# Performance work log

Hardware: AMD Instinct MI355X
Metric: run time of the kernel (lower is better)

## Reference

```python
import jax, jax.numpy as jnp
import numpy as np

B, T, D_IN, D_OUT = 4, 2048, 1024, 1024


def setup_inputs() -> dict:
    key = jax.random.key(0)
    k1, k2, k3, k4 = jax.random.split(key, 4)
    s_in = 1.0 / np.sqrt(D_IN)
    return {
        "input_vector": jax.random.normal(k1, (B, T, D_IN), dtype=jnp.float32),
        "w_q": jax.random.normal(k2, (D_IN, D_OUT), dtype=jnp.float32) * s_in,
        "w_k": jax.random.normal(k3, (D_IN, D_OUT), dtype=jnp.float32) * s_in,
        "w_v": jax.random.normal(k4, (D_IN, D_OUT), dtype=jnp.float32) * s_in,
    }


def reference(input_vector, w_q, w_k, w_v):
    # projections: [B, T, D_OUT]
    q = jnp.einsum("btd,de->bte", input_vector, w_q)
    k = jnp.einsum("btd,de->bte", input_vector, w_k)
    v = jnp.einsum("btd,de->bte", input_vector, w_v)

    T_ = q.shape[1]
    # raw scores [B, T, T]
    scores = jnp.einsum("bqd,bkd->bqk", q, k)
    # causal mask (strict upper triangle masked to -inf), applied BEFORE scaling
    # (as in the original; -inf is invariant under the scale anyway)
    causal = jnp.tril(jnp.ones((T_, T_), dtype=bool))  # True = keep
    scores = jnp.where(causal[None, :, :], scores, -jnp.inf)
    scores = scores / jnp.sqrt(jnp.asarray(k.shape[-1], scores.dtype))
    attn = jax.nn.softmax(scores, axis=-1)
    # dropout = 0.0 (eval): identity
    return jnp.einsum("bqk,bkd->bqd", attn, v)
```

## Files before the change

kernel.cpp:

```cpp
#include <hip/hip_runtime.h>
#include <cstdint>

typedef unsigned short u16;
typedef __attribute__((ext_vector_type(8))) short short8;
typedef __attribute__((ext_vector_type(16))) float f32x16;

__device__ __forceinline__ u16 f2bf(float f) {
  uint32_t u = __float_as_uint(f);
  u += 0x7FFFu + ((u >> 16) & 1u);
  return (u16)(u >> 16);
}

__device__ __forceinline__ void async_ld16(u16* lds, const u16* g) {
  __builtin_amdgcn_global_load_lds((const __attribute__((address_space(1))) uint32_t*)g,
                                   (__attribute__((address_space(3))) uint32_t*)lds,
                                   16, 0, 0);
}

__device__ __forceinline__ void lgkm0_fence() {
  asm volatile("s_waitcnt lgkmcnt(0)" ::: "memory");
  __builtin_amdgcn_sched_barrier(0);
}
__device__ __forceinline__ void vmw6_fence() {
  asm volatile("s_waitcnt vmcnt(6)" ::: "memory");
  __builtin_amdgcn_sched_barrier(0);
}
__device__ __forceinline__ void vmw0_fence() {
  asm volatile("s_waitcnt vmcnt(0)" ::: "memory");
  __builtin_amdgcn_sched_barrier(0);
}

#define MFMA32 __builtin_amdgcn_mfma_f32_32x32x16_bf16

template <int ROLE>
__global__ __launch_bounds__(512, 2) void g8(
    const u16* __restrict__ Xbf, const u16* __restrict__ Wt,
    u16* __restrict__ QK, u16* __restrict__ VtAll,
    u16* __restrict__ P, float* __restrict__ lpart)
{
  const int b = blockIdx.x;
  const int tid = threadIdx.x;
  const int lane = tid & 63;
  const int wave = tid >> 6;
  const int wr2 = wave >> 2;
  const int wc2 = wave & 3;
  const int m32 = lane & 31;
  const int hh = lane >> 5;

  __shared__ __align__(16) u16 ls[2][2][16384];

  const u16 *Abase, *Bh0, *Bh1;
  int m0, n0, zb = 0;
  bool scoresRole = false;

  if constexpr (ROLE == 0) {
    m0 = (b >> 3) * 256;
    n0 = (b & 7) * 128;
    Abase = Xbf;
    Bh0 = Wt;
    Bh1 = Wt + 1024L * 1024;
  } else {
    if (b < 144) {
      scoresRole = true;
      zb = b / 36;
      const int w = b - zb * 36;
      int mt = 0;
      while ((mt + 1) * (mt + 2) / 2 <= w) ++mt;
      const int nt = w - mt * (mt + 1) / 2;
      m0 = nt * 256;
      n0 = mt * 256;
      Abase = QK + 8192L * 1024 + (long)zb * 2048 * 1024;
      const u16* Bq = QK + (long)zb * 2048 * 1024;
      Bh0 = Bq; Bh1 = Bq;
    } else {
      const int v = b - 144;
      m0 = (v >> 5) * 256;
      n0 = (v & 31) * 256;
      Abase = Wt + 2L * 1024 * 1024;
      Bh0 = Xbf; Bh1 = Xbf;
    }
  }

  const int sr = tid >> 3, sg = tid & 7;
  const long swz = (long)((sg ^ (sr & 7)) * 8);
  const u16* pAst = Abase + (long)(m0 + sr) * 1024 + swz;
  const u16* pB[2];
  if constexpr (ROLE == 0) {
    pB[0] = Bh0 + (long)(n0 + sr) * 1024 + swz;
    pB[1] = Bh1 + (long)(n0 + sr) * 1024 + swz;
  } else {
    pB[0] = Bh0 + (long)(n0 + sr) * 1024 + swz;
    pB[1] = Bh0 + (long)(n0 + 128 + sr) * 1024 + swz;
  }

#define STG_A(bf, h, t_) do { \
    u16* _d = &ls[bf][0][(h) * 8192] + tid * 8; \
    const u16* _s = pAst + (long)(h) * 131072 + (long)(t_) * 64; \
    async_ld16(_d, _s); async_ld16(_d + 4096, _s + 65536); } while (0)
#define STG_B(bf, h, t_) do { \
    u16* _d = &ls[bf][1][(h) * 8192] + tid * 8; \
    const u16* _s = pB[h] + (long)(t_) * 64; \
    async_ld16(_d, _s); async_ld16(_d + 4096, _s + 65536); } while (0)

  int offAk[4], offBk[2][4];
#pragma unroll
  for (int ks = 0; ks < 4; ++ks) {
    const int kq = ((ks << 1) | hh) ^ (m32 & 7);
    offAk[ks] = (wr2 * 128 + m32) * 64 + kq * 8;
#pragma unroll
    for (int j = 0; j < 2; ++j) {
      const int rowB = (ROLE == 0) ? (j * 128 + wc2 * 32 + m32)
                                   : (wc2 * 64 + j * 32 + m32);
      offBk[j][ks] = rowB * 64 + kq * 8;
    }
  }

  f32x16 acc[4][2];
#pragma unroll
  for (int i = 0; i < 4; ++i)
#pragma unroll
    for (int j = 0; j < 2; ++j)
#pragma unroll
      for (int r = 0; r < 16; ++r) acc[i][j][r] = 0.f;

  STG_A(0, 0, 0); STG_A(0, 1, 0); STG_B(0, 0, 0); STG_B(0, 1, 0);
  STG_B(1, 0, 1); STG_B(1, 1, 1); STG_A(1, 0, 1);
  vmw6_fence();
  __builtin_amdgcn_s_barrier();

  short8 A0[4], A1[4], A2[4], A3[4], B0r[4], B1r[4];

#pragma unroll 1
  for (int t = 0; t < 16; ++t) {
    const u16* la = ls[t & 1][0];
    const u16* lb = ls[t & 1][1];

#pragma unroll
    for (int ks = 0; ks < 4; ++ks) {
      A0[ks]  = *(const short8*)&la[offAk[ks]];
      A1[ks]  = *(const short8*)&la[offAk[ks] + 2048];
      B0r[ks] = *(const short8*)&lb[offBk[0][ks]];
    }
    if (t < 15) STG_A((t + 1) & 1, 1, t + 1);
    __builtin_amdgcn_s_barrier();
    lgkm0_fence();
    __builtin_amdgcn_s_setprio(1);
#pragma unroll
    for (int ks = 0; ks < 4; ++ks) {
      acc[0][0] = MFMA32(A0[ks], B0r[ks], acc[0][0], 0, 0, 0);
      acc[1][0] = MFMA32(A1[ks], B0r[ks], acc[1][0], 0, 0, 0);
    }
    __builtin_amdgcn_s_setprio(0);
    __builtin_amdgcn_s_barrier();

#pragma unroll
    for (int ks = 0; ks < 4; ++ks)
      B1r[ks] = *(const short8*)&lb[offBk[1][ks]];
    __builtin_amdgcn_s_barrier();
    lgkm0_fence();
    __builtin_amdgcn_s_setprio(1);
#pragma unroll
    for (int ks = 0; ks < 4; ++ks) {
      acc[0][1] = MFMA32(A0[ks], B1r[ks], acc[0][1], 0, 0, 0);
      acc[1][1] = MFMA32(A1[ks], B1r[ks], acc[1][1], 0, 0, 0);
    }
    __builtin_amdgcn_s_setprio(0);
    __builtin_amdgcn_s_barrier();

#pragma unroll
    for (int ks = 0; ks < 4; ++ks) {
      A2[ks] = *(const short8*)&la[offAk[ks] + 4096];
      A3[ks] = *(const short8*)&la[offAk[ks] + 6144];
    }
    if (t < 14) STG_B(t & 1, 0, t + 2);
    __builtin_amdgcn_s_barrier();
    lgkm0_fence();
    __builtin_amdgcn_s_setprio(1);
#pragma unroll
    for (int ks = 0; ks < 4; ++ks) {
      acc[2][0] = MFMA32(A2[ks], B0r[ks], acc[2][0], 0, 0, 0);
      acc[3][0] = MFMA32(A3[ks], B0r[ks], acc[3][0], 0, 0, 0);
    }
    __builtin_amdgcn_s_setprio(0);
    __builtin_amdgcn_s_barrier();

    if (t < 14) { STG_B(t & 1, 1, t + 2); STG_A(t & 1, 0, t + 2); }
    __builtin_amdgcn_s_barrier();
    __builtin_amdgcn_s_setprio(1);
#pragma unroll
    for (int ks = 0; ks < 4; ++ks) {
      acc[2][1] = MFMA32(A2[ks], B1r[ks], acc[2][1], 0, 0, 0);
      acc[3][1] = MFMA32(A3[ks], B1r[ks], acc[3][1], 0, 0, 0);
    }
    __builtin_amdgcn_s_setprio(0);
    if (t < 14) vmw6_fence(); else vmw0_fence();
    __builtin_amdgcn_s_barrier();
  }
#undef STG_A
#undef STG_B

  const int ec = lane & 31;
  const int rb = hh * 4;

  if constexpr (ROLE == 0) {
#pragma unroll
    for (int j = 0; j < 2; ++j) {
      u16* Cj = QK + (long)j * 8192 * 1024;
      const int col = n0 + wc2 * 32 + ec;
#pragma unroll
      for (int i = 0; i < 4; ++i) {
        const int rbase = m0 + wr2 * 128 + i * 32 + rb;
#pragma unroll
        for (int r = 0; r < 16; ++r) {
          const int row = rbase + (r & 3) + 8 * (r >> 2);
          Cj[(long)row * 1024 + col] = f2bf(acc[i][j][r]);
        }
      }
    }
  } else if (scoresRole) {
    u16* Pp = P + (long)zb * 2048 * 2048;
    float* lpz = lpart + (long)zb * 16 * 2048;
    const int chunk = (m0 >> 7) + wr2;
#pragma unroll
    for (int j = 0; j < 2; ++j) {
      const int q = n0 + wc2 * 64 + j * 32 + ec;
      float s = 0.f;
#pragma unroll
      for (int i = 0; i < 4; ++i) {
        const int kb = m0 + wr2 * 128 + i * 32 + rb;
#pragma unroll
        for (int u = 0; u < 4; ++u) {
          const int k0r = kb + u * 8;
          float pv[4];
#pragma unroll
          for (int v = 0; v < 4; ++v) {
            float e = __expf(acc[i][j][u * 4 + v] * 0.03125f);
            if (k0r + v > q) e = 0.f;
            pv[v] = e;
            s += e;
          }
          ushort4 o;
          o.x = f2bf(pv[0]); o.y = f2bf(pv[1]);
          o.z = f2bf(pv[2]); o.w = f2bf(pv[3]);
          *(ushort4*)&Pp[(long)q * 2048 + k0r] = o;
        }
      }
      s += __shfl_xor(s, 32, 64);
      if (hh == 0) lpz[(long)chunk * 2048 + q] = s;
    }
  } else {
#pragma unroll
    for (int i = 0; i < 4; ++i) {
      const int rbase = m0 + wr2 * 128 + i * 32 + rb;
#pragma unroll
      for (int j = 0; j < 2; ++j) {
        const int col = n0 + wc2 * 64 + j * 32 + ec;
#pragma unroll
        for (int r = 0; r < 16; ++r) {
          const int row = rbase + (r & 3) + 8 * (r >> 2);
          VtAll[(long)row * 8192 + col] = f2bf(acc[i][j][r]);
        }
      }
    }
  }
}

__global__ __launch_bounds__(256) void pv(
    const u16* __restrict__ VtAll, const u16* __restrict__ P,
    const float* __restrict__ lpart, float* __restrict__ out)
{
  const int b = blockIdx.x;
  const int tid = threadIdx.x;
  const int lane = tid & 63;
  const int wave = tid >> 6;
  const int wr = (wave >> 1) * 64;
  const int wc = (wave & 1) * 32;

  __shared__ __align__(16) u16 lsa[2][4096];
  __shared__ __align__(16) u16 lsb[2][2048];
  __shared__ float l_s[128];

  const int zb = blockIdx.y;
  const int mb = 15 - (b >> 4);
  const int nb = b & 15;
  const int m0 = mb * 128;
  const int n0 = nb * 64;
  const int kmax = (mb + 1) * 128;

  const u16* A = P + (long)zb * 2048 * 2048;
  const u16* B = VtAll + (long)zb * 2048;

  const int c0 = tid, c1 = tid + 256;
  const int r0 = c0 >> 2, q0 = ((c0 & 3) ^ ((c0 >> 3) & 3)) * 8;
  const int r1 = c1 >> 2, q1 = ((c1 & 3) ^ ((c1 >> 3) & 3)) * 8;

  const int m32 = lane & 31;
  const int hh = lane >> 5;
  const int rsw = (m32 >> 1) & 3;
  int offA[2][2], offB[2];
#pragma unroll
  for (int ks = 0; ks < 2; ++ks) {
    const int kq = ((ks << 1) | hh) ^ rsw;
#pragma unroll
    for (int i = 0; i < 2; ++i)
      offA[i][ks] = (wr + i * 32 + m32) * 32 + kq * 8;
    offB[ks] = (wc + m32) * 32 + kq * 8;
  }

  const u16* pA0 = A + (long)(m0 + r0) * 2048 + q0;
  const u16* pA1 = A + (long)(m0 + r1) * 2048 + q1;
  const u16* pB0 = B + (long)(n0 + r0) * 8192 + q0;

  f32x16 acc[2];
#pragma unroll
  for (int i = 0; i < 2; ++i)
#pragma unroll
    for (int r = 0; r < 16; ++r) acc[i][r] = 0.f;

  async_ld16(&lsa[0][c0 * 8], pA0);
  async_ld16(&lsa[0][c1 * 8], pA1);
  async_ld16(&lsb[0][c0 * 8], pB0);
  pA0 += 32; pA1 += 32; pB0 += 32;

  int p = 0;
  for (int k0 = 0; k0 < kmax; k0 += 32) {
    __syncthreads();
    if (k0 + 32 < kmax) {
      async_ld16(&lsa[p ^ 1][c0 * 8], pA0);
      async_ld16(&lsa[p ^ 1][c1 * 8], pA1);
      async_ld16(&lsb[p ^ 1][c0 * 8], pB0);
      pA0 += 32; pA1 += 32; pB0 += 32;
    }
    const u16* la = lsa[p];
    const u16* lb = lsb[p];
#pragma unroll
    for (int ks = 0; ks < 2; ++ks) {
      const short8 a0 = *(const short8*)&la[offA[0][ks]];
      const short8 a1 = *(const short8*)&la[offA[1][ks]];
      const short8 bb = *(const short8*)&lb[offB[ks]];
      acc[0] = MFMA32(a0, bb, acc[0], 0, 0, 0);
      acc[1] = MFMA32(a1, bb, acc[1], 0, 0, 0);
    }
    p ^= 1;
  }

  __syncthreads();
  if (tid < 128) {
    const float* lp = lpart + (long)zb * 16 * 2048 + m0 + tid;
    float s = 0.f;
    const int nch = (mb | 1) + 1;
    for (int c = 0; c < nch; ++c) s += lp[(long)c * 2048];
    l_s[tid] = 1.f / s;
  }
  __syncthreads();

  const int ec = lane & 31;
  const int rb = hh * 4;
  float* Cf = out + (long)zb * 2048 * 1024;
#pragma unroll
  for (int i = 0; i < 2; ++i) {
    const int rbl = wr + i * 32 + rb;
    const int col = n0 + wc + ec;
#pragma unroll
    for (int r = 0; r < 16; ++r) {
      const int rl = rbl + (r & 3) + 8 * (r >> 2);
      Cf[(long)(m0 + rl) * 1024 + col] = acc[i][r] * l_s[rl];
    }
  }
}

__global__ __launch_bounds__(256) void cast_fused(
    const float* __restrict__ x, const float* __restrict__ w0,
    const float* __restrict__ w1, const float* __restrict__ w2,
    u16* __restrict__ Xbf, u16* __restrict__ Wt)
{
  const int b = blockIdx.x;
  if (b < 8192) {
    const long i = ((long)b * 256 + threadIdx.x) * 4;
    const float4 v = *(const float4*)(x + i);
    ushort4 o;
    o.x = f2bf(v.x); o.y = f2bf(v.y); o.z = f2bf(v.z); o.w = f2bf(v.w);
    *(ushort4*)(Xbf + i) = o;
  } else {
    const int bb = b - 8192;
    const int z = bb >> 10, rem = bb & 1023;
    const float* W = (z == 0) ? w0 : (z == 1) ? w1 : w2;
    u16* o = Wt + (long)z * 1024 * 1024;
    __shared__ float t[32][33];
    const int n0 = (rem & 31) * 32, k0 = (rem >> 5) * 32;
    const int tx = threadIdx.x & 31, ty = threadIdx.x >> 5;
    for (int r = ty; r < 32; r += 8) t[r][tx] = W[(long)(k0 + r) * 1024 + n0 + tx];
    __syncthreads();
    for (int r = ty; r < 32; r += 8) o[(long)(n0 + r) * 1024 + k0 + tx] = f2bf(t[tx][r]);
  }
}

extern "C" void kernel_launch(void* const* d_in, const int* in_sizes, int n_in,
                              void* d_out, int out_size, void* d_ws, size_t ws_size,
                              hipStream_t stream) {
  const float* X  = (const float*)d_in[0];
  const float* Wq = (const float*)d_in[1];
  const float* Wk = (const float*)d_in[2];
  const float* Wv = (const float*)d_in[3];
  float* out = (float*)d_out;

  u16* Xbf   = (u16*)d_ws;
  u16* Wt    = Xbf + 8192L * 1024;
  u16* QK    = Wt + 3L * 1024 * 1024;
  u16* VtAll = QK + 2L * 8192 * 1024;
  u16* P     = VtAll + 1024L * 8192;
  float* lpart = (float*)(P + 4L * 2048 * 2048);

  cast_fused<<<8192 + 3072, 256, 0, stream>>>(X, Wq, Wk, Wv, Xbf, Wt);

  g8<0><<<256, 512, 0, stream>>>(Xbf, Wt, QK, VtAll, P, lpart);

  g8<1><<<272, 512, 0, stream>>>(Xbf, Wt, QK, VtAll, P, lpart);

  pv<<<dim3(256, 4), 256, 0, stream>>>(VtAll, P, lpart, out);
}
```

Before: 258.3 us.

## Move V projection into QK launch and enlarge PV tiles with balanced pairing

The V-transpose projection moves out of the scores kernel into the first projection launch. It uses half-height 128-row tiles, giving 512 blocks there and leaving the scores launch with only the 144 causal tiles. The PV kernel switches from 128x64 tiles with k-steps of 32 to 128x128 tiles with k-steps of 64. Its grid now pairs long and short causal query tiles, so blocks issued early carry heavy work and later ones light work, cutting LDS traffic per MFMA and tail imbalance. The cost is more LDS and registers per PV block and a new pipelined code path with its own waitcnt accounting.

```diff
diff --git a/kernel.cpp b/kernel.cpp
--- a/kernel.cpp
+++ b/kernel.cpp
@@ -21,14 +21,8 @@
   asm volatile("s_waitcnt lgkmcnt(0)" ::: "memory");
   __builtin_amdgcn_sched_barrier(0);
 }
-__device__ __forceinline__ void vmw6_fence() {
-  asm volatile("s_waitcnt vmcnt(6)" ::: "memory");
-  __builtin_amdgcn_sched_barrier(0);
-}
-__device__ __forceinline__ void vmw0_fence() {
-  asm volatile("s_waitcnt vmcnt(0)" ::: "memory");
-  __builtin_amdgcn_sched_barrier(0);
-}
+#define VM_FENCE(N) do { asm volatile("s_waitcnt vmcnt(" #N ")" ::: "memory"); \
+                         __builtin_amdgcn_sched_barrier(0); } while (0)
 
 #define MFMA32 __builtin_amdgcn_mfma_f32_32x32x16_bf16
 
@@ -49,49 +43,45 @@
 
   __shared__ __align__(16) u16 ls[2][2][16384];
 
-  const u16 *Abase, *Bh0, *Bh1;
+  const u16 *Abase, *Brow0, *Brow1;
   int m0, n0, zb = 0;
-  bool scoresRole = false;
+  bool vthalf = false;
 
   if constexpr (ROLE == 0) {
-    m0 = (b >> 3) * 256;
-    n0 = (b & 7) * 128;
-    Abase = Xbf;
-    Bh0 = Wt;
-    Bh1 = Wt + 1024L * 1024;
-  } else {
-    if (b < 144) {
-      scoresRole = true;
-      zb = b / 36;
-      const int w = b - zb * 36;
-      int mt = 0;
-      while ((mt + 1) * (mt + 2) / 2 <= w) ++mt;
-      const int nt = w - mt * (mt + 1) / 2;
-      m0 = nt * 256;
-      n0 = mt * 256;
-      Abase = QK + 8192L * 1024 + (long)zb * 2048 * 1024;
-      const u16* Bq = QK + (long)zb * 2048 * 1024;
-      Bh0 = Bq; Bh1 = Bq;
+    if (b < 256) {
+      m0 = (b >> 3) * 256;
+      n0 = (b & 7) * 128;
+      Abase = Xbf;
+      Brow0 = Wt + (long)(n0)*1024;
+      Brow1 = Wt + 1024L * 1024 + (long)(n0)*1024;
     } else {
-      const int v = b - 144;
-      m0 = (v >> 5) * 256;
+      vthalf = true;
+      const int v = b - 256;
+      m0 = (v >> 5) * 128;
       n0 = (v & 31) * 256;
       Abase = Wt + 2L * 1024 * 1024;
-      Bh0 = Xbf; Bh1 = Xbf;
-    }
+      Brow0 = Xbf + (long)(n0)*1024;
+      Brow1 = Xbf + (long)(n0 + 128) * 1024;
+    }
+  } else {
+    zb = b / 36;
+    const int w = b - zb * 36;
+    int mt = 0;
+    while ((mt + 1) * (mt + 2) / 2 <= w) ++mt;
+    const int nt = w - mt * (mt + 1) / 2;
+    m0 = nt * 256;
+    n0 = mt * 256;
+    Abase = QK + 8192L * 1024 + (long)zb * 2048 * 1024;
+    const u16* Bq = QK + (long)zb * 2048 * 1024;
+    Brow0 = Bq + (long)(n0)*1024;
+    Brow1 = Bq + (long)(n0 + 128) * 1024;
   }
 
   const int sr = tid >> 3, sg = tid & 7;
   const long swz = (long)((sg ^ (sr & 7)) * 8);
   const u16* pAst = Abase + (long)(m0 + sr) * 1024 + swz;
-  const u16* pB[2];
-  if constexpr (ROLE == 0) {
-    pB[0] = Bh0 + (long)(n0 + sr) * 1024 + swz;
-    pB[1] = Bh1 + (long)(n0 + sr) * 1024 + swz;
-  } else {
-    pB[0] = Bh0 + (long)(n0 + sr) * 1024 + swz;
-    pB[1] = Bh0 + (long)(n0 + 128 + sr) * 1024 + swz;
-  }
+  const u16* pB[2] = { Brow0 + (long)sr * 1024 + swz,
+                       Brow1 + (long)sr * 1024 + swz };
 
 #define STG_A(bf, h, t_) do { \
     u16* _d = &ls[bf][0][(h) * 8192] + tid * 8; \
@@ -102,6 +92,94 @@
     const u16* _s = pB[h] + (long)(t_) * 64; \
     async_ld16(_d, _s); async_ld16(_d + 4096, _s + 65536); } while (0)
 
+  const int ec = lane & 31;
+  const int rb = hh * 4;
+
+  if constexpr (ROLE == 0) {
+    if (vthalf) {
+      int offAv[4], offBv[2][4];
+#pragma unroll
+      for (int ks = 0; ks < 4; ++ks) {
+        const int kq = ((ks << 1) | hh) ^ (m32 & 7);
+        offAv[ks] = (wr2 * 64 + m32) * 64 + kq * 8;
+#pragma unroll
+        for (int j = 0; j < 2; ++j)
+          offBv[j][ks] = (wc2 * 64 + j * 32 + m32) * 64 + kq * 8;
+      }
+
+      f32x16 acc[2][2];
+#pragma unroll
+      for (int i = 0; i < 2; ++i)
+#pragma unroll
+        for (int j = 0; j < 2; ++j)
+#pragma unroll
+          for (int r = 0; r < 16; ++r) acc[i][j][r] = 0.f;
+
+      STG_A(0, 0, 0); STG_B(0, 0, 0); STG_B(0, 1, 0);
+      VM_FENCE(0);
+      __builtin_amdgcn_s_barrier();
+
+      short8 A0[4], A1[4], B0r[4], B1r[4];
+
+#pragma unroll 1
+      for (int t = 0; t < 16; ++t) {
+        const u16* la = ls[t & 1][0];
+        const u16* lb = ls[t & 1][1];
+        const int nb = (t & 1) ^ 1;
+
+#pragma unroll
+        for (int ks = 0; ks < 4; ++ks) {
+          A0[ks]  = *(const short8*)&la[offAv[ks]];
+          A1[ks]  = *(const short8*)&la[offAv[ks] + 2048];
+          B0r[ks] = *(const short8*)&lb[offBv[0][ks]];
+        }
+        if (t < 15) { STG_A(nb, 0, t + 1); STG_B(nb, 0, t + 1); }
+        __builtin_amdgcn_s_barrier();
+        lgkm0_fence();
+        __builtin_amdgcn_s_setprio(1);
+#pragma unroll
+        for (int ks = 0; ks < 4; ++ks) {
+          acc[0][0] = MFMA32(A0[ks], B0r[ks], acc[0][0], 0, 0, 0);
+          acc[1][0] = MFMA32(A1[ks], B0r[ks], acc[1][0], 0, 0, 0);
+        }
+        __builtin_amdgcn_s_setprio(0);
+        if (t < 15) VM_FENCE(4); else VM_FENCE(0);
+        __builtin_amdgcn_s_barrier();
+
+#pragma unroll
+        for (int ks = 0; ks < 4; ++ks)
+          B1r[ks] = *(const short8*)&lb[offBv[1][ks]];
+        if (t < 15) STG_B(nb, 1, t + 1);
+        __builtin_amdgcn_s_barrier();
+        lgkm0_fence();
+        __builtin_amdgcn_s_setprio(1);
+#pragma unroll
+        for (int ks = 0; ks < 4; ++ks) {
+          acc[0][1] = MFMA32(A0[ks], B1r[ks], acc[0][1], 0, 0, 0);
+          acc[1][1] = MFMA32(A1[ks], B1r[ks], acc[1][1], 0, 0, 0);
+        }
+        __builtin_amdgcn_s_setprio(0);
+        if (t < 15) VM_FENCE(2); else VM_FENCE(0);
+        __builtin_amdgcn_s_barrier();
+      }
+
+#pragma unroll
+      for (int i = 0; i < 2; ++i) {
+        const int rbase = m0 + wr2 * 64 + i * 32 + rb;
+#pragma unroll
+        for (int j = 0; j < 2; ++j) {
+          const int col = n0 + wc2 * 64 + j * 32 + ec;
+#pragma unroll
+          for (int r = 0; r < 16; ++r) {
+            const int row = rbase + (r & 3) + 8 * (r >> 2);
+            VtAll[(long)row * 8192 + col] = f2bf(acc[i][j][r]);
+          }
+        }
+      }
+      return;
+    }
+  }
+
   int offAk[4], offBk[2][4];
 #pragma unroll
   for (int ks = 0; ks < 4; ++ks) {
@@ -125,7 +203,7 @@
 
   STG_A(0, 0, 0); STG_A(0, 1, 0); STG_B(0, 0, 0); STG_B(0, 1, 0);
   STG_B(1, 0, 1); STG_B(1, 1, 1); STG_A(1, 0, 1);
-  vmw6_fence();
+  VM_FENCE(6);
   __builtin_amdgcn_s_barrier();
 
   short8 A0[4], A1[4], A2[4], A3[4], B0r[4], B1r[4];
@@ -193,14 +271,11 @@
       acc[3][1] = MFMA32(A3[ks], B1r[ks], acc[3][1], 0, 0, 0);
     }
     __builtin_amdgcn_s_setprio(0);
-    if (t < 14) vmw6_fence(); else vmw0_fence();
+    if (t < 14) VM_FENCE(6); else VM_FENCE(0);
     __builtin_amdgcn_s_barrier();
   }
 #undef STG_A
 #undef STG_B
-
-  const int ec = lane & 31;
-  const int rb = hh * 4;
 
   if constexpr (ROLE == 0) {
 #pragma unroll
@@ -217,7 +292,7 @@
         }
       }
     }
-  } else if (scoresRole) {
+  } else {
     u16* Pp = P + (long)zb * 2048 * 2048;
     float* lpz = lpart + (long)zb * 16 * 2048;
     const int chunk = (m0 >> 7) + wr2;
@@ -231,36 +306,22 @@
 #pragma unroll
         for (int u = 0; u < 4; ++u) {
           const int k0r = kb + u * 8;
-          float pv[4];
+          float pv4[4];
 #pragma unroll
           for (int v = 0; v < 4; ++v) {
             float e = __expf(acc[i][j][u * 4 + v] * 0.03125f);
             if (k0r + v > q) e = 0.f;
-            pv[v] = e;
+            pv4[v] = e;
             s += e;
           }
           ushort4 o;
-          o.x = f2bf(pv[0]); o.y = f2bf(pv[1]);
-          o.z = f2bf(pv[2]); o.w = f2bf(pv[3]);
+          o.x = f2bf(pv4[0]); o.y = f2bf(pv4[1]);
+          o.z = f2bf(pv4[2]); o.w = f2bf(pv4[3]);
           *(ushort4*)&Pp[(long)q * 2048 + k0r] = o;
         }
       }
       s += __shfl_xor(s, 32, 64);
       if (hh == 0) lpz[(long)chunk * 2048 + q] = s;
-    }
-  } else {
-#pragma unroll
-    for (int i = 0; i < 4; ++i) {
-      const int rbase = m0 + wr2 * 128 + i * 32 + rb;
-#pragma unroll
-      for (int j = 0; j < 2; ++j) {
-        const int col = n0 + wc2 * 64 + j * 32 + ec;
-#pragma unroll
-        for (int r = 0; r < 16; ++r) {
-          const int row = rbase + (r & 3) + 8 * (r >> 2);
-          VtAll[(long)row * 8192 + col] = f2bf(acc[i][j][r]);
-        }
-      }
     }
   }
 }
@@ -273,83 +334,86 @@
   const int tid = threadIdx.x;
   const int lane = tid & 63;
   const int wave = tid >> 6;
-  const int wr = (wave >> 1) * 64;
-  const int wc = (wave & 1) * 32;
-
-  __shared__ __align__(16) u16 lsa[2][4096];
-  __shared__ __align__(16) u16 lsb[2][2048];
-  __shared__ float l_s[128];
-
-  const int zb = blockIdx.y;
-  const int mb = 15 - (b >> 4);
-  const int nb = b & 15;
-  const int m0 = mb * 128;
-  const int n0 = nb * 64;
-  const int kmax = (mb + 1) * 128;
-
-  const u16* A = P + (long)zb * 2048 * 2048;
-  const u16* B = VtAll + (long)zb * 2048;
-
-  const int c0 = tid, c1 = tid + 256;
-  const int r0 = c0 >> 2, q0 = ((c0 & 3) ^ ((c0 >> 3) & 3)) * 8;
-  const int r1 = c1 >> 2, q1 = ((c1 & 3) ^ ((c1 >> 3) & 3)) * 8;
-
+  const int wm = wave >> 1;
+  const int wn = wave & 1;
   const int m32 = lane & 31;
   const int hh = lane >> 5;
-  const int rsw = (m32 >> 1) & 3;
-  int offA[2][2], offB[2];
-#pragma unroll
-  for (int ks = 0; ks < 2; ++ks) {
-    const int kq = ((ks << 1) | hh) ^ rsw;
-#pragma unroll
-    for (int i = 0; i < 2; ++i)
-      offA[i][ks] = (wr + i * 32 + m32) * 32 + kq * 8;
-    offB[ks] = (wc + m32) * 32 + kq * 8;
-  }
-
-  const u16* pA0 = A + (long)(m0 + r0) * 2048 + q0;
-  const u16* pA1 = A + (long)(m0 + r1) * 2048 + q1;
-  const u16* pB0 = B + (long)(n0 + r0) * 8192 + q0;
-
-  f32x16 acc[2];
+
+  __shared__ __align__(16) u16 lsa[2][8192];
+  __shared__ __align__(16) u16 lsb[2][8192];
+  __shared__ float l_s[128];
+
+  const int id = b & 255;
+  const int zb = id >> 6;
+  const int r2 = id & 63;
+  const int dn = r2 >> 3;
+  const int pp = r2 & 7;
+  const int qt = (b < 256) ? (15 - pp) : pp;
+  const int m0 = qt * 128;
+  const int n0 = dn * 128;
+  const int nkt = (qt + 1) * 2;
+
+  const u16* Ab = P + (long)zb * 2048 * 2048;
+  const u16* Bb = VtAll + (long)zb * 2048;
+
+  const int prow = tid >> 3;
+  const long pswz = (long)(((tid & 7) ^ (prow & 7)) * 8);
+  const u16* pA = Ab + (long)(m0 + prow) * 2048 + pswz;
+  const u16* pB = Bb + (long)(n0 + prow) * 8192 + pswz;
+
+#define PV_STG(bf, t_) do { \
+    _Pragma("unroll") \
+    for (int jj = 0; jj < 4; ++jj) { \
+      async_ld16(&lsa[bf][(tid + jj * 256) * 8], pA + (long)jj * 32 * 2048 + (long)(t_) * 64); \
+      async_ld16(&lsb[bf][(tid + jj * 256) * 8], pB + (long)jj * 32 * 8192 + (long)(t_) * 64); \
+    } } while (0)
+
+  int offA[2][4], offB[2][4];
+#pragma unroll
+  for (int ks = 0; ks < 4; ++ks) {
+    const int kq = ((ks << 1) | hh) ^ (m32 & 7);
+#pragma unroll
+    for (int i = 0; i < 2; ++i) {
+      offA[i][ks] = (wm * 64 + i * 32 + m32) * 64 + kq * 8;
+      offB[i][ks] = (wn * 64 + i * 32 + m32) * 64 + kq * 8;
+    }
+  }
+
+  f32x16 acc[2][2];
 #pragma unroll
   for (int i = 0; i < 2; ++i)
 #pragma unroll
-    for (int r = 0; r < 16; ++r) acc[i][r] = 0.f;
-
-  async_ld16(&lsa[0][c0 * 8], pA0);
-  async_ld16(&lsa[0][c1 * 8], pA1);
-  async_ld16(&lsb[0][c0 * 8], pB0);
-  pA0 += 32; pA1 += 32; pB0 += 32;
-
-  int p = 0;
-  for (int k0 = 0; k0 < kmax; k0 += 32) {
+    for (int j = 0; j < 2; ++j)
+#pragma unroll
+      for (int r = 0; r < 16; ++r) acc[i][j][r] = 0.f;
+
+  PV_STG(0, 0);
+
+#pragma unroll 1
+  for (int t = 0; t < nkt; ++t) {
     __syncthreads();
-    if (k0 + 32 < kmax) {
-      async_ld16(&lsa[p ^ 1][c0 * 8], pA0);
-      async_ld16(&lsa[p ^ 1][c1 * 8], pA1);
-      async_ld16(&lsb[p ^ 1][c0 * 8], pB0);
-      pA0 += 32; pA1 += 32; pB0 += 32;
-    }
-    const u16* la = lsa[p];
-    const u16* lb = lsb[p];
-#pragma unroll
-    for (int ks = 0; ks < 2; ++ks) {
+    if (t + 1 < nkt) PV_STG((t & 1) ^ 1, t + 1);
+    const u16* la = lsa[t & 1];
+    const u16* lb = lsb[t & 1];
+#pragma unroll
+    for (int ks = 0; ks < 4; ++ks) {
       const short8 a0 = *(const short8*)&la[offA[0][ks]];
       const short8 a1 = *(const short8*)&la[offA[1][ks]];
-      const short8 bb = *(const short8*)&lb[offB[ks]];
-      acc[0] = MFMA32(a0, bb, acc[0], 0, 0, 0);
-      acc[1] = MFMA32(a1, bb, acc[1], 0, 0, 0);
-    }
-    p ^= 1;
-  }
+      const short8 b0 = *(const short8*)&lb[offB[0][ks]];
+      const short8 b1 = *(const short8*)&lb[offB[1][ks]];
+      acc[0][0] = MFMA32(a0, b0, acc[0][0], 0, 0, 0);
+      acc[0][1] = MFMA32(a0, b1, acc[0][1], 0, 0, 0);
+      acc[1][0] = MFMA32(a1, b0, acc[1][0], 0, 0, 0);
+      acc[1][1] = MFMA32(a1, b1, acc[1][1], 0, 0, 0);
+    }
+  }
+#undef PV_STG
 
   __syncthreads();
   if (tid < 128) {
     const float* lp = lpart + (long)zb * 16 * 2048 + m0 + tid;
     float s = 0.f;
-    const int nch = (mb | 1) + 1;
-    for (int c = 0; c < nch; ++c) s += lp[(long)c * 2048];
+    for (int c = 0; c <= qt; ++c) s += lp[(long)c * 2048];
     l_s[tid] = 1.f / s;
   }
   __syncthreads();
@@ -359,12 +423,15 @@
   float* Cf = out + (long)zb * 2048 * 1024;
 #pragma unroll
   for (int i = 0; i < 2; ++i) {
-    const int rbl = wr + i * 32 + rb;
-    const int col = n0 + wc + ec;
-#pragma unroll
-    for (int r = 0; r < 16; ++r) {
-      const int rl = rbl + (r & 3) + 8 * (r >> 2);
-      Cf[(long)(m0 + rl) * 1024 + col] = acc[i][r] * l_s[rl];
+    const int rbl = wm * 64 + i * 32 + rb;
+#pragma unroll
+    for (int j = 0; j < 2; ++j) {
+      const int col = n0 + wn * 64 + j * 32 + ec;
+#pragma unroll
+      for (int r = 0; r < 16; ++r) {
+        const int rl = rbl + (r & 3) + 8 * (r >> 2);
+        Cf[(long)(m0 + rl) * 1024 + col] = acc[i][j][r] * l_s[rl];
+      }
     }
   }
 }
@@ -413,9 +480,9 @@
 
   cast_fused<<<8192 + 3072, 256, 0, stream>>>(X, Wq, Wk, Wv, Xbf, Wt);
 
-  g8<0><<<256, 512, 0, stream>>>(Xbf, Wt, QK, VtAll, P, lpart);
-
-  g8<1><<<272, 512, 0, stream>>>(Xbf, Wt, QK, VtAll, P, lpart);
-
-  pv<<<dim3(256, 4), 256, 0, stream>>>(VtAll, P, lpart, out);
-}
+  g8<0><<<512, 512, 0, stream>>>(Xbf, Wt, QK, VtAll, P, lpart);
+
+  g8<1><<<144, 512, 0, stream>>>(Xbf, Wt, QK, VtAll, P, lpart);
+
+  pv<<<512, 256, 0, stream>>>(VtAll, P, lpart, out);
+}
```

After: 228.0 us. -11.7%, faster.
